# Kernel optimization log

Measured on AMD Instinct MI355X. Metric: run time of the kernel, lower is better.

## Reference

```python
import jax, jax.numpy as jnp
import numpy as np

N0, C1, C2 = 100000, 10000, 1000
E0 = 1_600_000
IN = 128
H = 128
OUT = 128


def _pool_edges(ei, ew, cluster, C):
    # PyG pool_edge: remap via cluster, drop self loops, coalesce (sum weights)
    m = cluster[ei]
    mask = m[0] != m[1]
    m = m[:, mask]
    w = ew[mask]
    keys = m[0] * C + m[1]
    uk, inv = np.unique(keys, return_inverse=True)
    w2 = np.bincount(inv, weights=w).astype(np.float32)
    return np.stack([uk // C, uk % C]).astype(np.int64), w2


def _with_self_loops(ei, ew, N):
    # gcn_norm(add_remaining_self_loops, fill_value=1); base edges have no loops
    row = np.concatenate([ei[0], np.arange(N)]).astype(np.int64)
    col = np.concatenate([ei[1], np.arange(N)]).astype(np.int64)
    w = np.concatenate([ew, np.ones(N, np.float32)])
    return row, col, w


def setup_inputs() -> dict:
    rng = np.random.default_rng(0)
    ei = rng.integers(0, N0, size=(2, E0))
    ei = ei[:, ei[0] != ei[1]]
    ew = np.ones(ei.shape[1], np.float32)
    # guaranteed-surjective cluster assignments (stand-in for Louvain output)
    c1 = rng.permutation(np.arange(N0) % C1).astype(np.int64)
    c2 = rng.permutation(np.arange(C1) % C2).astype(np.int64)
    ei1, ew1 = _pool_edges(ei, ew, c1, C1)
    ei2, ew2 = _pool_edges(ei1, ew1, c2, C2)
    r0, co0, w0 = _with_self_loops(ei, ew, N0)
    r1, co1, w1 = _with_self_loops(ei1, ew1, C1)
    r2, co2, w2 = _with_self_loops(ei2, ew2, C2)

    key = jax.random.key(0)
    ks = jax.random.split(key, 16)
    def lin(k, fi, fo):
        return jax.random.normal(k, (fi, fo), jnp.float32) / np.sqrt(fi)
    inp = {
        'x': jax.random.normal(ks[0], (N0, IN), jnp.float32),
        'W_pre': lin(ks[1], IN, H), 'b_pre': jnp.zeros((H,), jnp.float32),
        'W_u0': lin(ks[2], H, H), 'b_u0': jnp.zeros((H,), jnp.float32),
        'W_u1': lin(ks[3], H, H), 'b_u1': jnp.zeros((H,), jnp.float32),
        'W_u2': lin(ks[4], H, H), 'b_u2': jnp.zeros((H,), jnp.float32),
        'W_d0': lin(ks[5], H, OUT), 'b_d0': jnp.zeros((OUT,), jnp.float32),
        'W_d1': lin(ks[6], H, H), 'b_d1': jnp.zeros((H,), jnp.float32),
        'row0': jnp.asarray(r0), 'col0': jnp.asarray(co0), 'ew0': jnp.asarray(w0),
        'row1': jnp.asarray(r1), 'col1': jnp.asarray(co1), 'ew1': jnp.asarray(w1),
        'row2': jnp.asarray(r2), 'col2': jnp.asarray(co2), 'ew2': jnp.asarray(w2),
        'cluster1': jnp.asarray(c1), 'cluster2': jnp.asarray(c2),
    }
    return inp


def _gcn(x, W, b, row, col, ew, N):
    # PyG GCNConv: sym-normalized aggregation at target (col)
    deg = jax.ops.segment_sum(ew, col, num_segments=N)
    dinv = jnp.where(deg > 0, jax.lax.rsqrt(deg), 0.0)
    norm = dinv[row] * ew * dinv[col]
    h = x @ W                                   # [N, F_out]
    out = jax.ops.segment_sum(h[row] * norm[:, None], col, num_segments=N)
    return out + b


def _seg_mean(x, cluster, C):
    s = jax.ops.segment_sum(x, cluster, num_segments=C)
    cnt = jax.ops.segment_sum(jnp.ones((x.shape[0], 1), x.dtype), cluster,
                              num_segments=C)
    return s / jnp.maximum(cnt, 1.0)


def reference(x, W_pre, b_pre, W_u0, b_u0, W_u1, b_u1, W_u2, b_u2,
              W_d0, b_d0, W_d1, b_d1,
              row0, col0, ew0, row1, col1, ew1, row2, col2, ew2,
              cluster1, cluster2):
    # --- up (coarsening) path ---
    h = x @ W_pre + b_pre                                   # preembed
    x0 = jax.nn.relu(_gcn(h, W_u0, b_u0, row0, col0, ew0, N0))
    x1 = _seg_mean(x0, cluster1, C1)                        # avg_pool level 1
    x1 = jax.nn.relu(_gcn(x1, W_u1, b_u1, row1, col1, ew1, C1))
    x2 = _seg_mean(x1, cluster2, C2)                        # avg_pool level 2
    x2 = jax.nn.relu(_gcn(x2, W_u2, b_u2, row2, col2, ew2, C2))
    # --- down (unpooling) path; down convs use all-ones edge weights ---
    y = x1 + x2[cluster2]
    y = jax.nn.relu(_gcn(y, W_d1, b_d1, row1, col1, jnp.ones_like(ew1), C1))
    y = x0 + y[cluster1]
    y = _gcn(y, W_d0, b_d0, row0, col0, jnp.ones_like(ew0), N0)
    return y
```

## Files before the change

kernel.cpp:

```cpp
#include <hip/hip_runtime.h>

#define HH 128
static constexpr int kN0 = 100000;
static constexpr int kC1 = 10000;
static constexpr int kC2 = 1000;

static constexpr int B0 = kN0;
static constexpr int B1 = B0 + kC1;
static constexpr int B2 = B1 + kC2;
static constexpr int B3 = B2 + kC1;
static constexpr int NTOT = B3 + kC2;

static constexpr int NB0 = (kN0 + 127) / 128;
static constexpr int NB1 = (kC1 + 7) / 8;
static constexpr int NB2 = kC2;
static constexpr int NBP1 = (kC1 + 127) / 128;
static constexpr int NBP2 = (kC2 + 15) / 16;
static constexpr int Q0 = NB0;
static constexpr int Q1 = Q0 + NB1;
static constexpr int Q2 = Q1 + NB2;
static constexpr int Q3 = Q2 + NBP1;
static constexpr int NBK = Q3 + NBP2;

__device__ __forceinline__ int bucket_of(int bin) {
  if (bin < B0) return bin >> 7;
  if (bin < B1) return Q0 + ((bin - B0) >> 3);
  if (bin < B2) return Q1 + (bin - B1);
  if (bin < B3) return Q2 + ((bin - B2) >> 7);
  return Q3 + ((bin - B3) >> 4);
}

__device__ __forceinline__ unsigned int f2_to_bf2(float a, float b) {
  unsigned int ua = __float_as_uint(a);
  unsigned int ub = __float_as_uint(b);
  ua = (ua + 0x7fffu + ((ua >> 16) & 1u)) >> 16;
  ub = (ub + 0x7fffu + ((ub >> 16) & 1u)) & 0xffff0000u;
  return ua | ub;
}
__device__ __forceinline__ unsigned short f2bf(float f) {
  unsigned int u = __float_as_uint(f);
  u = (u + 0x7fffu + ((u >> 16) & 1u)) >> 16;
  return (unsigned short)u;
}
__device__ __forceinline__ float bf2f(unsigned short s) {
  return __uint_as_float(((unsigned int)s) << 16);
}

using bf16x8 = __attribute__((ext_vector_type(8))) short;
using f32x4 = __attribute__((ext_vector_type(4))) float;

__global__ __launch_bounds__(256) void p1_kernel(const int* __restrict__ col0,
                                                 const int* __restrict__ col1,
                                                 const int* __restrict__ col2,
                                                 const int* __restrict__ cl1,
                                                 const int* __restrict__ cl2,
                                                 int E0, int E1, int E2,
                                                 int* __restrict__ bucketCnt) {
  __shared__ int h[NBK];
  for (int i = threadIdx.x; i < NBK; i += 256) h[i] = 0;
  __syncthreads();
  int T0 = E0, T1 = T0 + E1, T2 = T1 + E2, T3 = T2 + kN0, T4 = T3 + kC1;
  for (int g = blockIdx.x * 256 + threadIdx.x; g < T4; g += gridDim.x * 256) {
    int bin;
    if (g < T0)      bin = col0[g];
    else if (g < T1) bin = B0 + col1[g - T0];
    else if (g < T2) bin = B1 + col2[g - T1];
    else if (g < T3) bin = B2 + cl1[g - T2];
    else             bin = B3 + cl2[g - T3];
    atomicAdd(&h[bucket_of(bin)], 1);
  }
  __syncthreads();
  for (int i = threadIdx.x; i < NBK; i += 256) {
    int c = h[i];
    if (c) atomicAdd(&bucketCnt[i], c);
  }
}

__global__ __launch_bounds__(1024) void p2_kernel(const int* __restrict__ bucketCnt,
                                                  int* __restrict__ bucketStart,
                                                  int* __restrict__ cursor,
                                                  int* __restrict__ startsg, int T) {
  int t = threadIdx.x;
  int v[4]; int s = 0;
#pragma unroll
  for (int j = 0; j < 4; j++) {
    int i = t * 4 + j;
    v[j] = (i < NBK) ? bucketCnt[i] : 0;
    s += v[j];
  }
  int lane = t & 63, w = t >> 6;
  int incl = s;
  for (int o = 1; o < 64; o <<= 1) { int u = __shfl_up(incl, o); if (lane >= o) incl += u; }
  __shared__ int wt[16];
  if (lane == 63) wt[w] = incl;
  __syncthreads();
  if (t == 0) { int run = 0; for (int i = 0; i < 16; i++) { int c = wt[i]; wt[i] = run; run += c; } }
  __syncthreads();
  int ex = wt[w] + incl - s;
#pragma unroll
  for (int j = 0; j < 4; j++) {
    int i = t * 4 + j;
    if (i < NBK) { bucketStart[i] = ex; cursor[i] = ex; }
    ex += v[j];
  }
  if (t == 0) { bucketStart[NBK] = T; startsg[NTOT] = T; }
}

__global__ __launch_bounds__(256) void p3_kernel(const int* __restrict__ col0,
                                                 const int* __restrict__ col1,
                                                 const int* __restrict__ col2,
                                                 const int* __restrict__ cl1,
                                                 const int* __restrict__ cl2,
                                                 const int* __restrict__ row0,
                                                 const int* __restrict__ row1,
                                                 const int* __restrict__ row2,
                                                 const float* __restrict__ ew1,
                                                 const float* __restrict__ ew2,
                                                 int E0, int E1, int E2,
                                                 int* __restrict__ cursor,
                                                 int4* __restrict__ part) {
  __shared__ int h[NBK];
  __shared__ int gbase[NBK];
  for (int i = threadIdx.x; i < NBK; i += 256) h[i] = 0;
  __syncthreads();
  int T0 = E0, T1 = T0 + E1, T2 = T1 + E2, T3 = T2 + kN0, T4 = T3 + kC1;
  int base = blockIdx.x * 4096;
  int bins[16], srcs[16], rk[16];
  float wv[16];
#pragma unroll
  for (int j = 0; j < 16; j++) {
    int g = base + threadIdx.x + j * 256;
    int bin = -1, src = 0; float w = 0.f;
    if (g < T4) {
      if (g < T0) { bin = col0[g]; src = row0[g]; }
      else if (g < T1) { int e = g - T0; bin = B0 + col1[e]; src = row1[e]; w = ew1[e]; }
      else if (g < T2) { int e = g - T1; bin = B1 + col2[e]; src = row2[e]; w = ew2[e]; }
      else if (g < T3) { int e = g - T2; bin = B2 + cl1[e]; src = e; }
      else             { int e = g - T3; bin = B3 + cl2[e]; src = e; }
    }
    bins[j] = bin; srcs[j] = src; wv[j] = w;
    rk[j] = (bin >= 0) ? atomicAdd(&h[bucket_of(bin)], 1) : 0;
  }
  __syncthreads();
  for (int i = threadIdx.x; i < NBK; i += 256) {
    int c = h[i];
    gbase[i] = c ? atomicAdd(&cursor[i], c) : 0;
  }
  __syncthreads();
#pragma unroll
  for (int j = 0; j < 16; j++) {
    if (bins[j] >= 0) {
      int slot = gbase[bucket_of(bins[j])] + rk[j];
      part[slot] = make_int4(bins[j], srcs[j], __float_as_int(wv[j]), 0);
    }
  }
}

__global__ __launch_bounds__(256) void p4_kernel(const int* __restrict__ bucketStart,
                                                 const int4* __restrict__ part,
                                                 int* __restrict__ startsg,
                                                 int* __restrict__ rowS,
                                                 float* __restrict__ ewSm) {
  int b = blockIdx.x;
  int binLo, width;
  if (b < Q0)      { binLo = b << 7;                 width = 128; if (binLo + width > B0) width = B0 - binLo; }
  else if (b < Q1) { binLo = B0 + ((b - Q0) << 3);   width = 8; }
  else if (b < Q2) { binLo = B1 + (b - Q1);          width = 1; }
  else if (b < Q3) { binLo = B2 + ((b - Q2) << 7);   width = 128; if (binLo + width > B3) width = B3 - binLo; }
  else             { binLo = B3 + ((b - Q3) << 4);   width = 16; if (binLo + width > NTOT) width = NTOT - binLo; }
  int base = bucketStart[b], nend = bucketStart[b + 1];
  int t = threadIdx.x;

  if (width == 1) {
    if (t == 0) startsg[binLo] = base;
    bool isEw = (binLo >= B0 && binLo < B2);
    for (int i = base + t; i < nend; i += 256) {
      int4 it = part[i];
      rowS[i] = it.y;
      if (isEw) ewSm[i] = __int_as_float(it.z);
    }
    return;
  }

  __shared__ int h[128];
  __shared__ int cur[128];
  if (t < 128) h[t] = 0;
  __syncthreads();
  for (int i = base + t; i < nend; i += 256) atomicAdd(&h[part[i].x - binLo], 1);
  __syncthreads();
  if (t == 0) {
    int run = 0;
    for (int j = 0; j < width; j++) {
      cur[j] = run;
      startsg[binLo + j] = base + run;
      run += h[j];
    }
  }
  __syncthreads();
  for (int i = base + t; i < nend; i += 256) {
    int4 it = part[i];
    int k = it.x;
    int r = atomicAdd(&cur[k - binLo], 1);
    int dst = base + r;
    rowS[dst] = it.y;
    if (k >= B0 && k < B2) ewSm[dst] = __int_as_float(it.z);
  }
}

__global__ void dinv_kernel(const int* __restrict__ startsg, const float* __restrict__ ewSm,
                            float* __restrict__ d0, float* __restrict__ d1w,
                            float* __restrict__ d1o, float* __restrict__ d2) {
  int t = blockIdx.x * 256 + threadIdx.x;
  if (t < kN0) {
    int c = startsg[t + 1] - startsg[t];
    d0[t] = c > 0 ? rsqrtf((float)c) : 0.f;
  }
  int wid = t >> 6, lane = t & 63;
  if (wid < kC1) {
    int s = startsg[B0 + wid], e = startsg[B0 + wid + 1];
    float a = 0.f;
    for (int k = s + lane; k < e; k += 64) a += ewSm[k];
    for (int o = 32; o > 0; o >>= 1) a += __shfl_down(a, o);
    if (lane == 0) {
      d1w[wid] = a > 0.f ? rsqrtf(a) : 0.f;
      int c = e - s;
      d1o[wid] = c > 0 ? rsqrtf((float)c) : 0.f;
    }
  } else if (wid < kC1 + kC2) {
    int w2 = wid - kC1;
    int s = startsg[B1 + w2], e = startsg[B1 + w2 + 1];
    float a = 0.f;
    for (int k = s + lane; k < e; k += 64) a += ewSm[k];
    for (int o = 32; o > 0; o >>= 1) a += __shfl_down(a, o);
    if (lane == 0) d2[w2] = a > 0.f ? rsqrtf(a) : 0.f;
  }
}

__global__ void wprep_kernel(const int* __restrict__ rowS, const float* __restrict__ ewSm,
                             const float* __restrict__ dinv0, const float* __restrict__ d1w,
                             const float* __restrict__ d1o, const float* __restrict__ d2,
                             int E0, int E1, int E2,
                             float* __restrict__ wAll, float* __restrict__ w1om) {
  int e = blockIdx.x * 256 + threadIdx.x;
  int tot = E0 + E1 + E2;
  if (e >= tot) return;
  int r = rowS[e];
  if (e < E0) {
    wAll[e] = dinv0[r];
  } else if (e < E0 + E1) {
    wAll[e] = d1w[r] * ewSm[e];
    w1om[e] = d1o[r];
  } else {
    wAll[e] = d2[r] * ewSm[e];
  }
}

__global__ __launch_bounds__(256) void matmul_kernel(const float* __restrict__ X,
                                                     const float* __restrict__ Xadd,
                                                     const int* __restrict__ cl,
                                                     const float* __restrict__ W,
                                                     const float* __restrict__ bias,
                                                     float* __restrict__ Y,
                                                     unsigned int* __restrict__ Ybf, int N) {
  __shared__ float Ws[64 * 128];
  __shared__ float Xs[32 * 128];
  int t = threadIdx.x;
  int rbase = blockIdx.x * 32;
  const float4* X4 = (const float4*)X;
  float4* Xs4 = (float4*)Xs;
#pragma unroll
  for (int i = 0; i < 4; i++) {
    int idx = t + 256 * i;
    int fr = idx >> 5, fc = idx & 31;
    int row = rbase + fr; if (row >= N) row = N - 1;
    float4 v = X4[(size_t)row * 32 + fc];
    if (Xadd) {
      int c = cl[row];
      float4 u = ((const float4*)Xadd)[(size_t)c * 32 + fc];
      v.x += u.x; v.y += u.y; v.z += u.z; v.w += u.w;
    }
    Xs4[idx] = v;
  }
  float acc[4][4];
#pragma unroll
  for (int r = 0; r < 4; r++)
#pragma unroll
    for (int cc = 0; cc < 4; cc++) acc[r][cc] = 0.f;
  int c0 = (t & 31) * 4;
  int rl = (t >> 5) * 4;
  const float4* W4 = (const float4*)W;
  float4* Ws4 = (float4*)Ws;
  for (int half = 0; half < 2; half++) {
    __syncthreads();
#pragma unroll
    for (int i = 0; i < 8; i++) {
      int idx = t + 256 * i;
      Ws4[idx] = W4[half * 2048 + idx];
    }
    __syncthreads();
#pragma unroll 4
    for (int k = 0; k < 64; k++) {
      float4 w4 = *(const float4*)(Ws + k * 128 + c0);
      float xv[4];
#pragma unroll
      for (int r = 0; r < 4; r++) xv[r] = Xs[(rl + r) * 128 + half * 64 + k];
#pragma unroll
      for (int r = 0; r < 4; r++) {
        acc[r][0] = fmaf(xv[r], w4.x, acc[r][0]);
        acc[r][1] = fmaf(xv[r], w4.y, acc[r][1]);
        acc[r][2] = fmaf(xv[r], w4.z, acc[r][2]);
        acc[r][3] = fmaf(xv[r], w4.w, acc[r][3]);
      }
    }
  }
  float4 b4 = make_float4(0.f, 0.f, 0.f, 0.f);
  if (bias) b4 = *(const float4*)(bias + c0);
#pragma unroll
  for (int r = 0; r < 4; r++) {
    int row = rbase + rl + r;
    if (row < N) {
      float4 o;
      o.x = acc[r][0] + b4.x; o.y = acc[r][1] + b4.y;
      o.z = acc[r][2] + b4.z; o.w = acc[r][3] + b4.w;
      if (Ybf) {
        unsigned int pk0 = f2_to_bf2(o.x, o.y);
        unsigned int pk1 = f2_to_bf2(o.z, o.w);
        *(uint2*)(Ybf + (size_t)row * 64 + (c0 >> 1)) = make_uint2(pk0, pk1);
      } else {
        *(float4*)(Y + (size_t)row * 128 + c0) = o;
      }
    }
  }
}

__global__ __launch_bounds__(256, 2) void mfma_gemm_kernel(
    const float* __restrict__ X, const float* __restrict__ Xadd,
    const int* __restrict__ cl, const float* __restrict__ W,
    const float* __restrict__ bias, unsigned int* __restrict__ Ybf, int N) {
  __shared__ unsigned int Bt[128 * 64];
  int t = threadIdx.x;
  {
    int n = t & 127, kh = t >> 7;
#pragma unroll
    for (int k = kh * 64; k < kh * 64 + 64; k += 2) {
      float a = W[(size_t)k * 128 + n];
      float b = W[(size_t)(k + 1) * 128 + n];
      unsigned int pk = (unsigned int)f2bf(a) | ((unsigned int)f2bf(b) << 16);
      unsigned int byteoff = ((unsigned int)(n * 256 + k * 2)) ^ (((unsigned int)n & 7u) << 4);
      *(unsigned int*)((char*)Bt + byteoff) = pk;
    }
  }
  __syncthreads();
  int wv = t >> 6, lane = t & 63;
  int g = lane >> 4, mrow = lane & 15;
  int rbase = blockIdx.x * 128 + wv * 32;
  bf16x8 ahi[2][4], alo[2][4];
#pragma unroll
  for (int mt = 0; mt < 2; mt++) {
    int row = rbase + mt * 16 + mrow;
    int rc = row < N ? row : N - 1;
    const float4* Xr = (const float4*)(X + (size_t)rc * 128);
    const float4* Ar = Xadd ? (const float4*)(Xadd + (size_t)cl[rc] * 128) : nullptr;
#pragma unroll
    for (int ks = 0; ks < 4; ks++) {
      int c4 = ks * 8 + g * 2;
      float4 v0 = Xr[c4], v1 = Xr[c4 + 1];
      if (Ar) {
        float4 u0 = Ar[c4], u1 = Ar[c4 + 1];
        v0.x += u0.x; v0.y += u0.y; v0.z += u0.z; v0.w += u0.w;
        v1.x += u1.x; v1.y += u1.y; v1.z += u1.z; v1.w += u1.w;
      }
      float vv[8] = {v0.x, v0.y, v0.z, v0.w, v1.x, v1.y, v1.z, v1.w};
      bf16x8 h, l;
#pragma unroll
      for (int j = 0; j < 8; j++) {
        unsigned short hb = f2bf(vv[j]);
        h[j] = (short)hb;
        l[j] = (short)f2bf(vv[j] - bf2f(hb));
      }
      ahi[mt][ks] = h; alo[mt][ks] = l;
    }
  }
  f32x4 acc[2][8];
#pragma unroll
  for (int mt = 0; mt < 2; mt++)
#pragma unroll
    for (int nt = 0; nt < 8; nt++) acc[mt][nt] = (f32x4){0.f, 0.f, 0.f, 0.f};
#pragma unroll
  for (int ks = 0; ks < 4; ks++) {
#pragma unroll
    for (int nt = 0; nt < 8; nt++) {
      int n = nt * 16 + mrow;
      unsigned int byteoff =
          ((unsigned int)(n * 256 + ks * 64 + g * 16)) ^ (((unsigned int)n & 7u) << 4);
      bf16x8 b = *(const bf16x8*)((const char*)Bt + byteoff);
      acc[0][nt] = __builtin_amdgcn_mfma_f32_16x16x32_bf16(ahi[0][ks], b, acc[0][nt], 0, 0, 0);
      acc[1][nt] = __builtin_amdgcn_mfma_f32_16x16x32_bf16(ahi[1][ks], b, acc[1][nt], 0, 0, 0);
      acc[0][nt] = __builtin_amdgcn_mfma_f32_16x16x32_bf16(alo[0][ks], b, acc[0][nt], 0, 0, 0);
      acc[1][nt] = __builtin_amdgcn_mfma_f32_16x16x32_bf16(alo[1][ks], b, acc[1][nt], 0, 0, 0);
    }
  }
#pragma unroll
  for (int mt = 0; mt < 2; mt++) {
#pragma unroll
    for (int r = 0; r < 4; r++) {
      int row = rbase + mt * 16 + g * 4 + r;
      if (row < N) {
#pragma unroll
        for (int nt = 0; nt < 4; nt++) {
          int c = nt * 16 + mrow;
          float lo = acc[mt][nt][r] + (bias ? bias[c] : 0.f);
          float hi = acc[mt][nt + 4][r] + (bias ? bias[c + 64] : 0.f);
          Ybf[(size_t)row * 64 + c] = (unsigned int)f2bf(lo) | ((unsigned int)f2bf(hi) << 16);
        }
      }
    }
  }
}

__global__ __launch_bounds__(256) void agg_kernel(const unsigned int* __restrict__ Hf,
                                                  float* __restrict__ out,
                                                  const int* __restrict__ starts,
                                                  const int* __restrict__ rowS,
                                                  const float* __restrict__ wS,
                                                  const float* __restrict__ dinv,
                                                  const float* __restrict__ bias,
                                                  int C, int relu) {
  int wid = (blockIdx.x * blockDim.x + threadIdx.x) >> 6;
  int lane = threadIdx.x & 63;
  if (wid >= C) return;
  int s = starts[wid], e = starts[wid + 1];
  float dc = dinv[wid];
  float ax[4] = {0.f, 0.f, 0.f, 0.f}, ay[4] = {0.f, 0.f, 0.f, 0.f};
  for (int base = s; base < e; base += 64) {
    int n = e - base; if (n > 64) n = 64;
    int moff = base + (lane < n ? lane : 0);
    int r = rowS[moff];
    float w = wS[moff];
    int j = 0;
    for (; j + 7 < n; j += 8) {
#pragma unroll
      for (int u = 0; u < 8; u++) {
        int rr = __shfl(r, j + u);
        float ww = __shfl(w, j + u);
        unsigned int pv = Hf[(size_t)rr * 64 + lane];
        ax[u & 3] = fmaf(ww, __uint_as_float(pv << 16), ax[u & 3]);
        ay[u & 3] = fmaf(ww, __uint_as_float(pv & 0xffff0000u), ay[u & 3]);
      }
    }
    for (; j < n; j++) {
      int rr = __shfl(r, j);
      float ww = __shfl(w, j);
      unsigned int pv = Hf[(size_t)rr * 64 + lane];
      ax[0] = fmaf(ww, __uint_as_float(pv << 16), ax[0]);
      ay[0] = fmaf(ww, __uint_as_float(pv & 0xffff0000u), ay[0]);
    }
  }
  float ox = (ax[0] + ax[1] + ax[2] + ax[3]) * dc + bias[lane];
  float oy = (ay[0] + ay[1] + ay[2] + ay[3]) * dc + bias[64 + lane];
  if (relu) { ox = fmaxf(ox, 0.f); oy = fmaxf(oy, 0.f); }
  out[(size_t)wid * 128 + lane] = ox;
  out[(size_t)wid * 128 + 64 + lane] = oy;
}

__global__ __launch_bounds__(256) void aggb_kernel(const unsigned int* __restrict__ Hf,
                                                   float* __restrict__ out,
                                                   const int* __restrict__ starts,
                                                   const int* __restrict__ rowS,
                                                   const float* __restrict__ wS,
                                                   const float* __restrict__ dinv,
                                                   const float* __restrict__ bias,
                                                   int C, int relu) {
  int node = blockIdx.x;
  if (node >= C) return;
  int wv = threadIdx.x >> 6, lane = threadIdx.x & 63;
  int s = starts[node], e = starts[node + 1];
  float ax[4] = {0.f, 0.f, 0.f, 0.f}, ay[4] = {0.f, 0.f, 0.f, 0.f};
  for (int base = s + wv * 64; base < e; base += 256) {
    int n = e - base; if (n > 64) n = 64;
    int moff = base + (lane < n ? lane : 0);
    int r = rowS[moff];
    float w = wS[moff];
    int j = 0;
    for (; j + 7 < n; j += 8) {
#pragma unroll
      for (int u = 0; u < 8; u++) {
        int rr = __shfl(r, j + u);
        float ww = __shfl(w, j + u);
        unsigned int pv = Hf[(size_t)rr * 64 + lane];
        ax[u & 3] = fmaf(ww, __uint_as_float(pv << 16), ax[u & 3]);
        ay[u & 3] = fmaf(ww, __uint_as_float(pv & 0xffff0000u), ay[u & 3]);
      }
    }
    for (; j < n; j++) {
      int rr = __shfl(r, j);
      float ww = __shfl(w, j);
      unsigned int pv = Hf[(size_t)rr * 64 + lane];
      ax[0] = fmaf(ww, __uint_as_float(pv << 16), ax[0]);
      ay[0] = fmaf(ww, __uint_as_float(pv & 0xffff0000u), ay[0]);
    }
  }
  __shared__ float shx[256], shy[256];
  shx[threadIdx.x] = ax[0] + ax[1] + ax[2] + ax[3];
  shy[threadIdx.x] = ay[0] + ay[1] + ay[2] + ay[3];
  __syncthreads();
  if (threadIdx.x < 64) {
    float sx = shx[lane] + shx[lane + 64] + shx[lane + 128] + shx[lane + 192];
    float sy = shy[lane] + shy[lane + 64] + shy[lane + 128] + shy[lane + 192];
    float dc = dinv[node];
    float ox = sx * dc + bias[lane * 2];
    float oy = sy * dc + bias[lane * 2 + 1];
    if (relu) { ox = fmaxf(ox, 0.f); oy = fmaxf(oy, 0.f); }
    *(float2*)(out + (size_t)node * 128 + lane * 2) = make_float2(ox, oy);
  }
}

__global__ __launch_bounds__(256) void pool_kernel(const float* __restrict__ src,
                                                   float* __restrict__ out,
                                                   const int* __restrict__ starts,
                                                   const int* __restrict__ rowS, int C) {
  int wid = (blockIdx.x * blockDim.x + threadIdx.x) >> 6;
  int lane = threadIdx.x & 63;
  if (wid >= C) return;
  int s = starts[wid], e = starts[wid + 1];
  float ax0 = 0.f, ay0 = 0.f, ax1 = 0.f, ay1 = 0.f;
  int m = s;
  for (; m + 3 < e; m += 4) {
    int i0 = rowS[m], i1 = rowS[m + 1], i2 = rowS[m + 2], i3 = rowS[m + 3];
    float2 v0 = *(const float2*)(src + (size_t)i0 * 128 + lane * 2);
    float2 v1 = *(const float2*)(src + (size_t)i1 * 128 + lane * 2);
    float2 v2 = *(const float2*)(src + (size_t)i2 * 128 + lane * 2);
    float2 v3 = *(const float2*)(src + (size_t)i3 * 128 + lane * 2);
    ax0 += v0.x; ay0 += v0.y;
    ax1 += v1.x; ay1 += v1.y;
    ax0 += v2.x; ay0 += v2.y;
    ax1 += v3.x; ay1 += v3.y;
  }
  for (; m < e; m++) {
    int id = rowS[m];
    const float2 v = *(const float2*)(src + (size_t)id * 128 + lane * 2);
    ax0 += v.x; ay0 += v.y;
  }
  float inv = (e > s) ? 1.f / (float)(e - s) : 0.f;
  *(float2*)(out + (size_t)wid * 128 + lane * 2) =
      make_float2((ax0 + ax1) * inv, (ay0 + ay1) * inv);
}


extern "C" void kernel_launch(void* const* d_in, const int* in_sizes, int n_in,
                              void* d_out, int out_size, void* d_ws, size_t ws_size,
                              hipStream_t stream) {
  const float* x     = (const float*)d_in[0];
  const float* W_pre = (const float*)d_in[1];
  const float* b_pre = (const float*)d_in[2];
  const float* W_u0  = (const float*)d_in[3];
  const float* b_u0  = (const float*)d_in[4];
  const float* W_u1  = (const float*)d_in[5];
  const float* b_u1  = (const float*)d_in[6];
  const float* W_u2  = (const float*)d_in[7];
  const float* b_u2  = (const float*)d_in[8];
  const float* W_d0  = (const float*)d_in[9];
  const float* b_d0  = (const float*)d_in[10];
  const float* W_d1  = (const float*)d_in[11];
  const float* b_d1  = (const float*)d_in[12];
  const int* row0 = (const int*)d_in[13];
  const int* col0 = (const int*)d_in[14];
  const int* row1 = (const int*)d_in[16];
  const int* col1 = (const int*)d_in[17];
  const float* ew1 = (const float*)d_in[18];
  const int* row2 = (const int*)d_in[19];
  const int* col2 = (const int*)d_in[20];
  const float* ew2 = (const float*)d_in[21];
  const int* cluster1 = (const int*)d_in[22];
  const int* cluster2 = (const int*)d_in[23];
  int E0 = in_sizes[13], E1 = in_sizes[16], E2 = in_sizes[19];
  float* out = (float*)d_out;
  int Ttot = E0 + E1 + E2 + kN0 + kC1;
  int Etot = E0 + E1 + E2;

  char* basep = (char*)d_ws;
  size_t off = 0;
  auto alloc = [&](size_t bytes) -> char* {
    char* p = basep + off;
    off = (off + bytes + 255) & ~(size_t)255;
    return p;
  };
  int* bucketCnt = (int*)alloc((size_t)NBK * 4);
  size_t zero_bytes = off;
  int* bucketStart = (int*)alloc((size_t)(NBK + 1) * 4);
  int* cursor      = (int*)alloc((size_t)NBK * 4);
  int* startsg     = (int*)alloc((size_t)(NTOT + 1) * 4);
  int* rowS  = (int*)alloc((size_t)Ttot * 4);
  float* ewS = (float*)alloc((size_t)(E1 + E2) * 4);
  float* ewSm = ewS - E0;
  float* dinv0  = (float*)alloc((size_t)kN0 * 4);
  float* dinv1w = (float*)alloc((size_t)kC1 * 4);
  float* dinv1o = (float*)alloc((size_t)kC1 * 4);
  float* dinv2  = (float*)alloc((size_t)kC2 * 4);
  size_t watermark = off;
  int4* part = (int4*)alloc((size_t)Ttot * 16);
  off = watermark;
  float* wAll = (float*)alloc((size_t)Etot * 4);
  float* w1o  = (float*)alloc((size_t)E1 * 4);
  float* w1om = w1o - E0;
  float* Wf   = (float*)alloc((size_t)128 * 128 * 4);
  float* bfv  = (float*)alloc((size_t)128 * 4);
  float* A    = (float*)alloc((size_t)kN0 * HH * 4);
  float* s1a  = (float*)alloc((size_t)kC1 * HH * 4);
  float* s1b  = (float*)alloc((size_t)kC1 * HH * 4);
  float* s2a  = (float*)alloc((size_t)kC2 * HH * 4);
  unsigned int* s1bb = (unsigned int*)alloc((size_t)kC1 * 64 * 4);
  unsigned int* s2bb = (unsigned int*)alloc((size_t)kC2 * 64 * 4);
  unsigned int* s1cb = (unsigned int*)alloc((size_t)kC1 * 64 * 4);
  unsigned int* tb   = (unsigned int*)alloc((size_t)kN0 * 64 * 4);
  unsigned int* t0   = (unsigned int*)d_out;

  hipMemsetAsync(d_ws, 0, zero_bytes, stream);

  auto cdiv = [](int a, int b) { return (a + b - 1) / b; };

  p1_kernel<<<256, 256, 0, stream>>>(col0, col1, col2, cluster1, cluster2, E0, E1, E2, bucketCnt);
  p2_kernel<<<1, 1024, 0, stream>>>(bucketCnt, bucketStart, cursor, startsg, Ttot);
  p3_kernel<<<cdiv(Ttot, 4096), 256, 0, stream>>>(col0, col1, col2, cluster1, cluster2,
                                                  row0, row1, row2, ew1, ew2, E0, E1, E2,
                                                  cursor, part);
  p4_kernel<<<NBK, 256, 0, stream>>>(bucketStart, part, startsg, rowS, ewSm);
  dinv_kernel<<<cdiv((kC1 + kC2) * 64, 256), 256, 0, stream>>>(startsg, ewSm, dinv0, dinv1w,
                                                               dinv1o, dinv2);
  wprep_kernel<<<cdiv(Etot, 256), 256, 0, stream>>>(rowS, ewSm, dinv0, dinv1w, dinv1o, dinv2,
                                                    E0, E1, E2, wAll, w1om);

  matmul_kernel<<<cdiv(128, 32), 256, 0, stream>>>(W_pre, nullptr, nullptr, W_u0, nullptr,
                                                   Wf, nullptr, 128);
  matmul_kernel<<<1, 256, 0, stream>>>(b_pre, nullptr, nullptr, W_u0, nullptr,
                                       bfv, nullptr, 1);
  mfma_gemm_kernel<<<cdiv(kN0, 128), 256, 0, stream>>>(x, nullptr, nullptr, Wf, bfv, t0, kN0);
  agg_kernel<<<cdiv(kN0, 4), 256, 0, stream>>>(t0, A, startsg, rowS, wAll, dinv0, b_u0, kN0, 1);
  pool_kernel<<<cdiv(kC1, 4), 256, 0, stream>>>(A, s1a, startsg + B2, rowS, kC1);
  matmul_kernel<<<cdiv(kC1, 32), 256, 0, stream>>>(s1a, nullptr, nullptr, W_u1, nullptr,
                                                   nullptr, s1bb, kC1);
  aggb_kernel<<<kC1, 256, 0, stream>>>(s1bb, s1a, startsg + B0, rowS, wAll, dinv1w, b_u1, kC1, 1);
  pool_kernel<<<cdiv(kC2, 4), 256, 0, stream>>>(s1a, s2a, startsg + B3, rowS, kC2);
  matmul_kernel<<<cdiv(kC2, 32), 256, 0, stream>>>(s2a, nullptr, nullptr, W_u2, nullptr,
                                                   nullptr, s2bb, kC2);
  aggb_kernel<<<kC2, 256, 0, stream>>>(s2bb, s2a, startsg + B1, rowS, wAll, dinv2, b_u2, kC2, 1);
  matmul_kernel<<<cdiv(kC1, 32), 256, 0, stream>>>(s1a, s2a, cluster2, W_d1, nullptr,
                                                   nullptr, s1cb, kC1);
  aggb_kernel<<<kC1, 256, 0, stream>>>(s1cb, s1b, startsg + B0, rowS, w1om, dinv1o, b_d1, kC1, 1);
  mfma_gemm_kernel<<<cdiv(kN0, 128), 256, 0, stream>>>(A, s1b, cluster1, W_d0, nullptr, tb, kN0);
  agg_kernel<<<cdiv(kN0, 4), 256, 0, stream>>>(tb, out, startsg, rowS, wAll, dinv0, b_d0, kN0, 0);
}
```

Baseline: 677.9 us.

## Fold source-node degree normalization into GEMM epilogue, drop per-edge weight loads

For the unit-weight GCN layers (level 0 both directions, level 1 down), the source-side D^-1/2 factor is now applied per row in the GEMM epilogue before the bf16 store. Aggregation kernels can then sum neighbour rows without loading or shuffling per-edge weights. wprep no longer writes the level-0 and level-1-ones weight arrays. This removes a large per-edge weight array read in the two big N0 aggregations and most of wprep's traffic, at the cost of rounding pre-scaled values to bf16.

```diff
diff --git a/kernel.cpp b/kernel.cpp
--- a/kernel.cpp
+++ b/kernel.cpp
@@ -237,19 +237,15 @@
 }
 
 __global__ void wprep_kernel(const int* __restrict__ rowS, const float* __restrict__ ewSm,
-                             const float* __restrict__ dinv0, const float* __restrict__ d1w,
-                             const float* __restrict__ d1o, const float* __restrict__ d2,
+                             const float* __restrict__ d1w, const float* __restrict__ d2,
                              int E0, int E1, int E2,
-                             float* __restrict__ wAll, float* __restrict__ w1om) {
-  int e = blockIdx.x * 256 + threadIdx.x;
+                             float* __restrict__ wAll) {
+  int e = blockIdx.x * 256 + threadIdx.x + E0;
   int tot = E0 + E1 + E2;
   if (e >= tot) return;
   int r = rowS[e];
-  if (e < E0) {
-    wAll[e] = dinv0[r];
-  } else if (e < E0 + E1) {
+  if (e < E0 + E1) {
     wAll[e] = d1w[r] * ewSm[e];
-    w1om[e] = d1o[r];
   } else {
     wAll[e] = d2[r] * ewSm[e];
   }
@@ -260,6 +256,7 @@
                                                      const int* __restrict__ cl,
                                                      const float* __restrict__ W,
                                                      const float* __restrict__ bias,
+                                                     const float* __restrict__ rowScale,
                                                      float* __restrict__ Y,
                                                      unsigned int* __restrict__ Ybf, int N) {
   __shared__ float Ws[64 * 128];
@@ -319,9 +316,10 @@
   for (int r = 0; r < 4; r++) {
     int row = rbase + rl + r;
     if (row < N) {
+      float sc = rowScale ? rowScale[row] : 1.f;
       float4 o;
-      o.x = acc[r][0] + b4.x; o.y = acc[r][1] + b4.y;
-      o.z = acc[r][2] + b4.z; o.w = acc[r][3] + b4.w;
+      o.x = (acc[r][0] + b4.x) * sc; o.y = (acc[r][1] + b4.y) * sc;
+      o.z = (acc[r][2] + b4.z) * sc; o.w = (acc[r][3] + b4.w) * sc;
       if (Ybf) {
         unsigned int pk0 = f2_to_bf2(o.x, o.y);
         unsigned int pk1 = f2_to_bf2(o.z, o.w);
@@ -336,7 +334,8 @@
 __global__ __launch_bounds__(256, 2) void mfma_gemm_kernel(
     const float* __restrict__ X, const float* __restrict__ Xadd,
     const int* __restrict__ cl, const float* __restrict__ W,
-    const float* __restrict__ bias, unsigned int* __restrict__ Ybf, int N) {
+    const float* __restrict__ bias, const float* __restrict__ rowScale,
+    unsigned int* __restrict__ Ybf, int N) {
   __shared__ unsigned int Bt[128 * 64];
   int t = threadIdx.x;
   {
@@ -406,11 +405,12 @@
     for (int r = 0; r < 4; r++) {
       int row = rbase + mt * 16 + g * 4 + r;
       if (row < N) {
+        float sc = rowScale ? rowScale[row] : 1.f;
 #pragma unroll
         for (int nt = 0; nt < 4; nt++) {
           int c = nt * 16 + mrow;
-          float lo = acc[mt][nt][r] + (bias ? bias[c] : 0.f);
-          float hi = acc[mt][nt + 4][r] + (bias ? bias[c + 64] : 0.f);
+          float lo = (acc[mt][nt][r] + (bias ? bias[c] : 0.f)) * sc;
+          float hi = (acc[mt][nt + 4][r] + (bias ? bias[c + 64] : 0.f)) * sc;
           Ybf[(size_t)row * 64 + c] = (unsigned int)f2bf(lo) | ((unsigned int)f2bf(hi) << 16);
         }
       }
@@ -422,7 +422,6 @@
                                                   float* __restrict__ out,
                                                   const int* __restrict__ starts,
                                                   const int* __restrict__ rowS,
-                                                  const float* __restrict__ wS,
                                                   const float* __restrict__ dinv,
                                                   const float* __restrict__ bias,
                                                   int C, int relu) {
@@ -434,26 +433,22 @@
   float ax[4] = {0.f, 0.f, 0.f, 0.f}, ay[4] = {0.f, 0.f, 0.f, 0.f};
   for (int base = s; base < e; base += 64) {
     int n = e - base; if (n > 64) n = 64;
-    int moff = base + (lane < n ? lane : 0);
-    int r = rowS[moff];
-    float w = wS[moff];
+    int r = rowS[base + (lane < n ? lane : 0)];
     int j = 0;
     for (; j + 7 < n; j += 8) {
 #pragma unroll
       for (int u = 0; u < 8; u++) {
         int rr = __shfl(r, j + u);
-        float ww = __shfl(w, j + u);
         unsigned int pv = Hf[(size_t)rr * 64 + lane];
-        ax[u & 3] = fmaf(ww, __uint_as_float(pv << 16), ax[u & 3]);
-        ay[u & 3] = fmaf(ww, __uint_as_float(pv & 0xffff0000u), ay[u & 3]);
+        ax[u & 3] += __uint_as_float(pv << 16);
+        ay[u & 3] += __uint_as_float(pv & 0xffff0000u);
       }
     }
     for (; j < n; j++) {
       int rr = __shfl(r, j);
-      float ww = __shfl(w, j);
       unsigned int pv = Hf[(size_t)rr * 64 + lane];
-      ax[0] = fmaf(ww, __uint_as_float(pv << 16), ax[0]);
-      ay[0] = fmaf(ww, __uint_as_float(pv & 0xffff0000u), ay[0]);
+      ax[0] += __uint_as_float(pv << 16);
+      ay[0] += __uint_as_float(pv & 0xffff0000u);
     }
   }
   float ox = (ax[0] + ax[1] + ax[2] + ax[3]) * dc + bias[lane];
@@ -498,6 +493,53 @@
       unsigned int pv = Hf[(size_t)rr * 64 + lane];
       ax[0] = fmaf(ww, __uint_as_float(pv << 16), ax[0]);
       ay[0] = fmaf(ww, __uint_as_float(pv & 0xffff0000u), ay[0]);
+    }
+  }
+  __shared__ float shx[256], shy[256];
+  shx[threadIdx.x] = ax[0] + ax[1] + ax[2] + ax[3];
+  shy[threadIdx.x] = ay[0] + ay[1] + ay[2] + ay[3];
+  __syncthreads();
+  if (threadIdx.x < 64) {
+    float sx = shx[lane] + shx[lane + 64] + shx[lane + 128] + shx[lane + 192];
+    float sy = shy[lane] + shy[lane + 64] + shy[lane + 128] + shy[lane + 192];
+    float dc = dinv[node];
+    float ox = sx * dc + bias[lane * 2];
+    float oy = sy * dc + bias[lane * 2 + 1];
+    if (relu) { ox = fmaxf(ox, 0.f); oy = fmaxf(oy, 0.f); }
+    *(float2*)(out + (size_t)node * 128 + lane * 2) = make_float2(ox, oy);
+  }
+}
+
+__global__ __launch_bounds__(256) void aggb1_kernel(const unsigned int* __restrict__ Hf,
+                                                    float* __restrict__ out,
+                                                    const int* __restrict__ starts,
+                                                    const int* __restrict__ rowS,
+                                                    const float* __restrict__ dinv,
+                                                    const float* __restrict__ bias,
+                                                    int C, int relu) {
+  int node = blockIdx.x;
+  if (node >= C) return;
+  int wv = threadIdx.x >> 6, lane = threadIdx.x & 63;
+  int s = starts[node], e = starts[node + 1];
+  float ax[4] = {0.f, 0.f, 0.f, 0.f}, ay[4] = {0.f, 0.f, 0.f, 0.f};
+  for (int base = s + wv * 64; base < e; base += 256) {
+    int n = e - base; if (n > 64) n = 64;
+    int r = rowS[base + (lane < n ? lane : 0)];
+    int j = 0;
+    for (; j + 7 < n; j += 8) {
+#pragma unroll
+      for (int u = 0; u < 8; u++) {
+        int rr = __shfl(r, j + u);
+        unsigned int pv = Hf[(size_t)rr * 64 + lane];
+        ax[u & 3] += __uint_as_float(pv << 16);
+        ay[u & 3] += __uint_as_float(pv & 0xffff0000u);
+      }
+    }
+    for (; j < n; j++) {
+      int rr = __shfl(r, j);
+      unsigned int pv = Hf[(size_t)rr * 64 + lane];
+      ax[0] += __uint_as_float(pv << 16);
+      ay[0] += __uint_as_float(pv & 0xffff0000u);
     }
   }
   __shared__ float shx[256], shy[256];
@@ -601,8 +643,6 @@
   int4* part = (int4*)alloc((size_t)Ttot * 16);
   off = watermark;
   float* wAll = (float*)alloc((size_t)Etot * 4);
-  float* w1o  = (float*)alloc((size_t)E1 * 4);
-  float* w1om = w1o - E0;
   float* Wf   = (float*)alloc((size_t)128 * 128 * 4);
   float* bfv  = (float*)alloc((size_t)128 * 4);
   float* A    = (float*)alloc((size_t)kN0 * HH * 4);
@@ -627,26 +667,28 @@
   p4_kernel<<<NBK, 256, 0, stream>>>(bucketStart, part, startsg, rowS, ewSm);
   dinv_kernel<<<cdiv((kC1 + kC2) * 64, 256), 256, 0, stream>>>(startsg, ewSm, dinv0, dinv1w,
                                                                dinv1o, dinv2);
-  wprep_kernel<<<cdiv(Etot, 256), 256, 0, stream>>>(rowS, ewSm, dinv0, dinv1w, dinv1o, dinv2,
-                                                    E0, E1, E2, wAll, w1om);
+  wprep_kernel<<<cdiv(E1 + E2, 256), 256, 0, stream>>>(rowS, ewSm, dinv1w, dinv2,
+                                                       E0, E1, E2, wAll);
 
   matmul_kernel<<<cdiv(128, 32), 256, 0, stream>>>(W_pre, nullptr, nullptr, W_u0, nullptr,
-                                                   Wf, nullptr, 128);
+                                                   nullptr, Wf, nullptr, 128);
   matmul_kernel<<<1, 256, 0, stream>>>(b_pre, nullptr, nullptr, W_u0, nullptr,
-                                       bfv, nullptr, 1);
-  mfma_gemm_kernel<<<cdiv(kN0, 128), 256, 0, stream>>>(x, nullptr, nullptr, Wf, bfv, t0, kN0);
-  agg_kernel<<<cdiv(kN0, 4), 256, 0, stream>>>(t0, A, startsg, rowS, wAll, dinv0, b_u0, kN0, 1);
+                                       nullptr, bfv, nullptr, 1);
+  mfma_gemm_kernel<<<cdiv(kN0, 128), 256, 0, stream>>>(x, nullptr, nullptr, Wf, bfv, dinv0,
+                                                       t0, kN0);
+  agg_kernel<<<cdiv(kN0, 4), 256, 0, stream>>>(t0, A, startsg, rowS, dinv0, b_u0, kN0, 1);
   pool_kernel<<<cdiv(kC1, 4), 256, 0, stream>>>(A, s1a, startsg + B2, rowS, kC1);
   matmul_kernel<<<cdiv(kC1, 32), 256, 0, stream>>>(s1a, nullptr, nullptr, W_u1, nullptr,
-                                                   nullptr, s1bb, kC1);
+                                                   nullptr, nullptr, s1bb, kC1);
   aggb_kernel<<<kC1, 256, 0, stream>>>(s1bb, s1a, startsg + B0, rowS, wAll, dinv1w, b_u1, kC1, 1);
   pool_kernel<<<cdiv(kC2, 4), 256, 0, stream>>>(s1a, s2a, startsg + B3, rowS, kC2);
   matmul_kernel<<<cdiv(kC2, 32), 256, 0, stream>>>(s2a, nullptr, nullptr, W_u2, nullptr,
-                                                   nullptr, s2bb, kC2);
+                                                   nullptr, nullptr, s2bb, kC2);
   aggb_kernel<<<kC2, 256, 0, stream>>>(s2bb, s2a, startsg + B1, rowS, wAll, dinv2, b_u2, kC2, 1);
   matmul_kernel<<<cdiv(kC1, 32), 256, 0, stream>>>(s1a, s2a, cluster2, W_d1, nullptr,
-                                                   nullptr, s1cb, kC1);
-  aggb_kernel<<<kC1, 256, 0, stream>>>(s1cb, s1b, startsg + B0, rowS, w1om, dinv1o, b_d1, kC1, 1);
-  mfma_gemm_kernel<<<cdiv(kN0, 128), 256, 0, stream>>>(A, s1b, cluster1, W_d0, nullptr, tb, kN0);
-  agg_kernel<<<cdiv(kN0, 4), 256, 0, stream>>>(tb, out, startsg, rowS, wAll, dinv0, b_d0, kN0, 0);
-}
+                                                   dinv1o, nullptr, s1cb, kC1);
+  aggb1_kernel<<<kC1, 256, 0, stream>>>(s1cb, s1b, startsg + B0, rowS, dinv1o, b_d1, kC1, 1);
+  mfma_gemm_kernel<<<cdiv(kN0, 128), 256, 0, stream>>>(A, s1b, cluster1, W_d0, nullptr, dinv0,
+                                                       tb, kN0);
+  agg_kernel<<<cdiv(kN0, 4), 256, 0, stream>>>(tb, out, startsg, rowS, dinv0, b_d0, kN0, 0);
+}
```

Result: faster. 660.5 us (-2.6%).
